# Kernel tuning notes

Hardware: AMD Instinct MI355X
Metric: run time of the kernel (lower is better)

## Reference

```python
import jax, jax.numpy as jnp
import numpy as np

HEAD_NUM = 8
NEG = 10000.0


def setup_inputs() -> dict:
    key = jax.random.key(0)
    ks = jax.random.split(key, 8)
    B, S, D = 2, 2048, 512
    sc = 1.0 / np.sqrt(D)
    return {
        "x": jax.random.normal(ks[0], (B, S, D), dtype=jnp.float32),
        "mask": jax.random.randint(ks[1], (B, S), 0, 2, dtype=jnp.int32),
        "Wq": jax.random.normal(ks[2], (D, D), dtype=jnp.float32) * sc,
        "bq": jnp.zeros((D,), jnp.float32),
        "Wk": jax.random.normal(ks[3], (D, D), dtype=jnp.float32) * sc,
        "bk": jnp.zeros((D,), jnp.float32),
        "Wv": jax.random.normal(ks[4], (D, D), dtype=jnp.float32) * sc,
        "bv": jnp.zeros((D,), jnp.float32),
        "Wo": jax.random.normal(ks[5], (D, D), dtype=jnp.float32) * sc,
        "bo": jnp.zeros((D,), jnp.float32),
    }


def _split_heads(t, H):
    B, S, D = t.shape
    return t.reshape(B, S, H, D // H).transpose(0, 2, 1, 3)  # [B,H,S,hd]


def reference(x, mask, Wq, bq, Wk, bk, Wv, bv, Wo, bo):
    B, S, D = x.shape
    H = HEAD_NUM
    hd = D // H
    # linear projections + relu activation (as in keras layer)
    q = jax.nn.relu(x @ Wq + bq)
    k = jax.nn.relu(x @ Wk + bk)
    v = jax.nn.relu(x @ Wv + bv)
    q = _split_heads(q, H)
    k = _split_heads(k, H)
    v = _split_heads(v, H)
    # scaled dot-product scores: scale by sqrt(head_dim) (query last dim after split)
    e = jnp.einsum("bhqd,bhkd->bhqk", q, k) / jnp.sqrt(jnp.float32(hd))
    # causal (history_only) additive mask
    idx = jnp.arange(S)
    causal = (idx[None, :] > idx[:, None]).astype(jnp.float32)  # [S,S]
    e = e - NEG * causal[None, None, :, :]
    # key padding mask, additive
    e = e - NEG * (1.0 - mask.astype(jnp.float32))[:, None, None, :]
    # stable softmax (explicit max-subtract as in source)
    a = jax.nn.softmax(e, axis=-1)
    out = jnp.einsum("bhqk,bhkd->bhqd", a, v)  # [B,H,S,hd]
    out = out.transpose(0, 2, 1, 3).reshape(B, S, D)
    # output projection + activation
    return jax.nn.relu(out @ Wo + bo)
```

## Files before the change

kernel.cpp:

```cpp
#include <hip/hip_runtime.h>
#include <hip/hip_bf16.h>

constexpr int Bc = 2, Sc = 2048, Dc = 512, Hc = 8, HDc = 64;
constexpr int Mtot = Bc * Sc;
constexpr size_t HEADMAT = (size_t)Bc * Hc * Sc * HDc;
constexpr float SC2  = 0.18033688011112042f;
constexpr float NEG2 = 14426.950408889634f;

typedef __attribute__((ext_vector_type(8)))  short          short8;
typedef __attribute__((ext_vector_type(8)))  unsigned short ushort8;
typedef __attribute__((ext_vector_type(4)))  float          f32x4;
typedef __attribute__((ext_vector_type(16))) float          f32x16;

#define MFMA16 __builtin_amdgcn_mfma_f32_16x16x32_bf16
#define MFMA32 __builtin_amdgcn_mfma_f32_32x32x16_bf16

static __device__ __forceinline__ unsigned short f32_to_bf16_bits(float f) {
    unsigned int u = __builtin_bit_cast(unsigned int, f);
    unsigned int r = u + 0x7FFFu + ((u >> 16) & 1u);
    return (unsigned short)(r >> 16);
}
static __device__ __forceinline__ unsigned int pkbf(float a, float b) {
    return (unsigned int)f32_to_bf16_bits(a) |
           ((unsigned int)f32_to_bf16_bits(b) << 16);
}

__global__ __launch_bounds__(256)
void convert_x(const float* __restrict__ x, unsigned short* __restrict__ Xb, int n)
{
    const int i = (blockIdx.x * 256 + threadIdx.x) * 4;
    if (i >= n) return;
    const float4 v = *(const float4*)(x + i);
    ushort4 o;
    o.x = f32_to_bf16_bits(v.x);
    o.y = f32_to_bf16_bits(v.y);
    o.z = f32_to_bf16_bits(v.z);
    o.w = f32_to_bf16_bits(v.w);
    *(ushort4*)(Xb + i) = o;
}

__global__ __launch_bounds__(256)
void transpose_w(const float* __restrict__ W0, const float* __restrict__ W1,
                 const float* __restrict__ W2, const float* __restrict__ W3,
                 unsigned short* __restrict__ Wt)
{
    __shared__ float T[64][65];
    const int z = blockIdx.z;
    const float* Wp = (z == 0) ? W0 : (z == 1) ? W1 : (z == 2) ? W2 : W3;
    unsigned short* Op = Wt + (size_t)z * 512 * 512;

    const int kt = blockIdx.y * 64, nt = blockIdx.x * 64;
    const int t = threadIdx.x;
    const int r  = t >> 2, c4 = (t & 3) * 16;

    #pragma unroll
    for (int i = 0; i < 4; ++i) {
        const float4 v = *(const float4*)(Wp + (size_t)(kt + r) * 512 + nt + c4 + 4 * i);
        T[r][c4 + 4*i + 0] = v.x;
        T[r][c4 + 4*i + 1] = v.y;
        T[r][c4 + 4*i + 2] = v.z;
        T[r][c4 + 4*i + 3] = v.w;
    }
    __syncthreads();

    const int n = t >> 2, k4 = (t & 3) * 16;
    #pragma unroll
    for (int i = 0; i < 4; ++i) {
        ushort4 o;
        o.x = f32_to_bf16_bits(T[k4 + 4*i + 0][n]);
        o.y = f32_to_bf16_bits(T[k4 + 4*i + 1][n]);
        o.z = f32_to_bf16_bits(T[k4 + 4*i + 2][n]);
        o.w = f32_to_bf16_bits(T[k4 + 4*i + 3][n]);
        *(ushort4*)(Op + (size_t)(nt + n) * 512 + kt + k4 + 4 * i) = o;
    }
}

template<bool HEADOUT>
__global__ __launch_bounds__(256)
void gemm_tile(const unsigned short* __restrict__ Xb,
               const unsigned short* __restrict__ Wt,
               const float* __restrict__ b0, const float* __restrict__ b1,
               const float* __restrict__ b2,
               unsigned short* __restrict__ Hout,
               float* __restrict__ Yf)
{
    __shared__ short As[128 * 32];
    __shared__ short Bs[64 * 32];

    const int lane = threadIdx.x & 63, wave = threadIdx.x >> 6;
    const int c = lane & 15, g = lane >> 4;
    const int wr = wave >> 1, wc = wave & 1;
    const int z = blockIdx.z;
    const unsigned short* Wp = Wt + (size_t)z * 512 * 512;
    const float* bp = (z == 0) ? b0 : (z == 1) ? b1 : b2;
    const int bm = blockIdx.y * 128;
    const int bn = blockIdx.x * 64;

    const int srow = lane >> 2;
    const int scol = (lane & 3) * 8;

    f32x4 acc[4][2] = {};

    for (int k0 = 0; k0 < 512; k0 += 32) {
        __syncthreads();
        #pragma unroll
        for (int i = 0; i < 2; ++i) {
            const int row = (wave * 2 + i) * 16 + srow;
            const short8 v = *(const short8*)(Xb + (size_t)(bm + row) * 512 + k0 + scol);
            *(short8*)(&As[row * 32 + scol]) = v;
        }
        {
            const int row = wave * 16 + srow;
            const short8 v = *(const short8*)(Wp + (size_t)(bn + row) * 512 + k0 + scol);
            *(short8*)(&Bs[row * 32 + scol]) = v;
        }
        __syncthreads();

        short8 a[4], bfr[2];
        #pragma unroll
        for (int mi = 0; mi < 4; ++mi)
            a[mi] = *(const short8*)(&As[(wr * 64 + mi * 16 + c) * 32 + g * 8]);
        #pragma unroll
        for (int ni = 0; ni < 2; ++ni)
            bfr[ni] = *(const short8*)(&Bs[(wc * 32 + ni * 16 + c) * 32 + g * 8]);
        #pragma unroll
        for (int mi = 0; mi < 4; ++mi)
            #pragma unroll
            for (int ni = 0; ni < 2; ++ni)
                acc[mi][ni] = MFMA16(a[mi], bfr[ni], acc[mi][ni], 0, 0, 0);
    }

    #pragma unroll
    for (int mi = 0; mi < 4; ++mi) {
        #pragma unroll
        for (int ni = 0; ni < 2; ++ni) {
            const int n = bn + wc * 32 + ni * 16 + c;
            const float bias = bp[n];
            float v[4];
            #pragma unroll
            for (int r = 0; r < 4; ++r)
                v[r] = fmaxf(acc[mi][ni][r] + bias, 0.0f);
            const int mbase = bm + wr * 64 + mi * 16 + 4 * g;
            if constexpr (HEADOUT) {
                const int bb = mbase >> 11, ss = mbase & 2047;
                const int hh = n >> 6, hd = n & 63;
                if (z == 2) {
                    union { ushort4 u; unsigned short s[4]; } pk;
                    #pragma unroll
                    for (int r = 0; r < 4; ++r) pk.s[r] = f32_to_bf16_bits(v[r]);
                    *reinterpret_cast<ushort4*>(
                        Hout + (size_t)2 * HEADMAT +
                        ((size_t)(bb * Hc + hh) * HDc + hd) * Sc + ss) = pk.u;
                } else {
                    #pragma unroll
                    for (int r = 0; r < 4; ++r)
                        Hout[(size_t)z * HEADMAT +
                             (((size_t)(bb * Hc + hh) * Sc + ss + r) * HDc + hd)] =
                            f32_to_bf16_bits(v[r]);
                }
            } else {
                #pragma unroll
                for (int r = 0; r < 4; ++r)
                    Yf[(size_t)(mbase + r) * 512 + n] = v[r];
            }
        }
    }
}

__global__ __launch_bounds__(256)
void attn_mfma(const short* __restrict__ Qh, const short* __restrict__ Kh,
               const short* __restrict__ Vt, const int* __restrict__ mask,
               unsigned short* __restrict__ Ob)
{
    __shared__ __align__(16) char smem[4 * 8448 + 4 * 256];

    const int lane = threadIdx.x & 63;
    const int wave = threadIdx.x >> 6;
    const int bid  = blockIdx.x;
    const int swz  = (bid & 7) * 128 + (bid >> 3);
    const int t    = swz & 63;
    const int h    = (swz >> 6) & 7;
    const int b    = swz >> 9;
    const int q0   = t * 32;
    const int r32  = lane & 31;
    const int hi   = lane >> 5;

    char*  wreg = smem + wave * 8448;
    float* Lml  = (float*)(smem + 4 * 8448 + wave * 256);

    const size_t headoff = (size_t)(b * Hc + h) * Sc * HDc;
    const short* Qp = Qh + headoff;
    const short* Kp = Kh + headoff;
    const short* Vp = Vt + headoff;
    const int* mb = mask + b * Sc;

    int fb = Sc;
    for (int base = 0; base < Sc; base += 64) {
        unsigned long long bal = __ballot(mb[base + lane] != 0);
        if (bal) { fb = base + (__ffsll(bal) - 1); break; }
    }
    const int kmax = (fb <= q0) ? (q0 + 32) : Sc;
    const int kend = (kmax + 31) & ~31;
    const int nT   = kend >> 5;
    const int tpw  = (nT + 3) >> 2;
    const int kbeg = wave * tpw * 32;
    const int kfin = min(kend, kbeg + tpw * 32);

    short8 qf[4];
    #pragma unroll
    for (int j = 0; j < 4; ++j)
        qf[j] = *(const short8*)(Qp + (size_t)(q0 + r32) * HDc + j * 16 + hi * 8);

    f32x16 acc0 = {0,0,0,0,0,0,0,0,0,0,0,0,0,0,0,0};
    f32x16 acc1 = {0,0,0,0,0,0,0,0,0,0,0,0,0,0,0,0};
    float m = -1e30f, l = 0.0f;

    const short* vrow0 = Vp + (size_t)r32 * Sc + 8 * hi;
    const short* vrow1 = Vp + (size_t)(32 + r32) * Sc + 8 * hi;

    for (int k0 = kbeg; k0 < kfin; k0 += 32) {
        const short8 va0 = *(const short8*)(vrow0 + k0);
        const short8 va1 = *(const short8*)(vrow0 + k0 + 16);
        const short8 vb0 = *(const short8*)(vrow1 + k0);
        const short8 vb1 = *(const short8*)(vrow1 + k0 + 16);

        f32x16 s = {0,0,0,0,0,0,0,0,0,0,0,0,0,0,0,0};
        #pragma unroll
        for (int j = 0; j < 4; ++j) {
            const short8 kf =
                *(const short8*)(Kp + (size_t)(k0 + r32) * HDc + j * 16 + hi * 8);
            s = MFMA32(kf, qf[j], s, 0, 0, 0);
        }

        const unsigned long long bal = __ballot(mb[k0 + r32] != 0);
        const unsigned int mloc = ((unsigned int)bal) >> (4 * hi);

        float e[16];
        float tmax = -1e30f;
        if (k0 + 31 > q0) {
            #pragma unroll
            for (int r = 0; r < 16; ++r) {
                const int cr0 = (r & 3) + 8 * (r >> 2);
                float ev = s[r] * SC2;
                if (!((mloc >> cr0) & 1))            ev -= NEG2;
                if (k0 + cr0 + 4 * hi > q0 + r32)    ev -= NEG2;
                e[r] = ev;
                tmax = fmaxf(tmax, ev);
            }
        } else {
            #pragma unroll
            for (int r = 0; r < 16; ++r) {
                const int cr0 = (r & 3) + 8 * (r >> 2);
                float ev = s[r] * SC2;
                if (!((mloc >> cr0) & 1))            ev -= NEG2;
                e[r] = ev;
                tmax = fmaxf(tmax, ev);
            }
        }
        tmax = fmaxf(tmax, __shfl_xor(tmax, 32));

        if (__any(tmax > m)) {
            const float mn   = fmaxf(m, tmax);
            const float corr = __builtin_exp2f(m - mn);
            m = mn; l *= corr;
            acc0 *= corr;
            acc1 *= corr;
        }

        float ps = 0.f;
        #pragma unroll
        for (int r = 0; r < 16; ++r) {
            e[r] = __builtin_exp2f(e[r] - m);
            ps += e[r];
        }
        l += ps;

        const unsigned int A0 = pkbf(e[0],  e[1]),  B0 = pkbf(e[2],  e[3]);
        const unsigned int C0 = pkbf(e[4],  e[5]),  D0 = pkbf(e[6],  e[7]);
        const unsigned int A1 = pkbf(e[8],  e[9]),  B1 = pkbf(e[10], e[11]);
        const unsigned int C1 = pkbf(e[12], e[13]), D1 = pkbf(e[14], e[15]);
        const unsigned int A0s = (unsigned int)__shfl_xor((int)A0, 32);
        const unsigned int B0s = (unsigned int)__shfl_xor((int)B0, 32);
        const unsigned int C0s = (unsigned int)__shfl_xor((int)C0, 32);
        const unsigned int D0s = (unsigned int)__shfl_xor((int)D0, 32);
        const unsigned int A1s = (unsigned int)__shfl_xor((int)A1, 32);
        const unsigned int B1s = (unsigned int)__shfl_xor((int)B1, 32);
        const unsigned int C1s = (unsigned int)__shfl_xor((int)C1, 32);
        const unsigned int D1s = (unsigned int)__shfl_xor((int)D1, 32);

        union { unsigned int u[4]; short8 s8; } P0, P1;
        P0.u[0] = hi ? C0s : A0;  P0.u[1] = hi ? D0s : B0;
        P0.u[2] = hi ? C0  : A0s; P0.u[3] = hi ? D0  : B0s;
        P1.u[0] = hi ? C1s : A1;  P1.u[1] = hi ? D1s : B1;
        P1.u[2] = hi ? C1  : A1s; P1.u[3] = hi ? D1  : B1s;

        acc0 = MFMA32(va0, P0.s8, acc0, 0, 0, 0);
        acc0 = MFMA32(va1, P1.s8, acc0, 0, 0, 0);
        acc1 = MFMA32(vb0, P0.s8, acc1, 0, 0, 0);
        acc1 = MFMA32(vb1, P1.s8, acc1, 0, 0, 0);
    }

    l += __shfl_xor(l, 32);

    {
        float* Lacc = (float*)wreg;
        #pragma unroll
        for (int r = 0; r < 16; ++r) {
            Lacc[lane * 33 + r]      = acc0[r];
            Lacc[lane * 33 + 16 + r] = acc1[r];
        }
        if (lane < 32) { Lml[lane] = m; Lml[32 + lane] = l; }
    }
    __syncthreads();

    float mu[4], lu[4], M = -1e30f;
    #pragma unroll
    for (int u = 0; u < 4; ++u) {
        const float* LmlU = (const float*)(smem + 4 * 8448 + u * 256);
        mu[u] = LmlU[r32];
        lu[u] = LmlU[32 + r32];
        M = fmaxf(M, mu[u]);
    }
    float wgt[4], L = 0.f;
    #pragma unroll
    for (int u = 0; u < 4; ++u) {
        wgt[u] = __builtin_exp2f(mu[u] - M);
        L += wgt[u] * lu[u];
    }
    const float invL = 1.0f / L;

    #pragma unroll
    for (int jj = 0; jj < 8; ++jj) {
        const int j = wave * 8 + jj;
        float o = 0.f;
        #pragma unroll
        for (int u = 0; u < 4; ++u)
            o += wgt[u] * ((const float*)(smem + u * 8448))[lane * 33 + j];
        const int j16 = j & 15;
        const int d = (j16 & 3) + 8 * (j16 >> 2) + 4 * hi + 32 * (j >> 4);
        Ob[(size_t)(b * Sc + q0 + r32) * Dc + h * HDc + d] =
            f32_to_bf16_bits(o * invL);
    }
}

extern "C" void kernel_launch(void* const* d_in, const int* in_sizes, int n_in,
                              void* d_out, int out_size, void* d_ws, size_t ws_size,
                              hipStream_t stream) {
    const float* x  = (const float*)d_in[0];
    const int* mask = (const int*)d_in[1];
    const float* Wq = (const float*)d_in[2];
    const float* bq = (const float*)d_in[3];
    const float* Wk = (const float*)d_in[4];
    const float* bk = (const float*)d_in[5];
    const float* Wv = (const float*)d_in[6];
    const float* bv = (const float*)d_in[7];
    const float* Wo = (const float*)d_in[8];
    const float* bo = (const float*)d_in[9];
    float* out = (float*)d_out;

    unsigned short* Xb = (unsigned short*)d_ws;
    unsigned short* Wt = Xb + (size_t)Mtot * 512;
    unsigned short* Qh = Wt + (size_t)4 * 512 * 512;
    unsigned short* Kh = Qh + HEADMAT;
    unsigned short* Vt = Kh + HEADMAT;
    unsigned short* Ob = Vt + HEADMAT;

    convert_x<<<dim3((Mtot * 512) / 1024), dim3(256), 0, stream>>>(
        x, Xb, Mtot * 512);
    transpose_w<<<dim3(8, 8, 4), dim3(256), 0, stream>>>(Wq, Wk, Wv, Wo, Wt);
    gemm_tile<true><<<dim3(8, Mtot / 128, 3), dim3(256), 0, stream>>>(
        Xb, Wt, bq, bk, bv, Qh, nullptr);
    attn_mfma<<<dim3(1024), dim3(256), 0, stream>>>(
        (const short*)Qh, (const short*)Kh, (const short*)Vt, mask, Ob);
    gemm_tile<false><<<dim3(8, Mtot / 128, 1), dim3(256), 0, stream>>>(
        Ob, Wt + (size_t)3 * 512 * 512, bo, bo, bo, nullptr, out);
}
```

Measured before the change: 97.49 us.

## Panelize V layout, prescale Q, reverse tile order, use packed bf16 convert

Measured after the change: 92.87 us. 1.05x faster.

```diff
diff --git a/kernel.cpp b/kernel.cpp
--- a/kernel.cpp
+++ b/kernel.cpp
@@ -20,9 +20,10 @@
     unsigned int r = u + 0x7FFFu + ((u >> 16) & 1u);
     return (unsigned short)(r >> 16);
 }
-static __device__ __forceinline__ unsigned int pkbf(float a, float b) {
-    return (unsigned int)f32_to_bf16_bits(a) |
-           ((unsigned int)f32_to_bf16_bits(b) << 16);
+static __device__ __forceinline__ unsigned int pk2bf(float a, float b) {
+    union { __hip_bfloat162 h2; unsigned int u; } cv;
+    cv.h2 = __float22bfloat162_rn(make_float2(a, b));
+    return cv.u;
 }
 
 __global__ __launch_bounds__(256)
@@ -138,8 +139,10 @@
             const float bias = bp[n];
             float v[4];
             #pragma unroll
-            for (int r = 0; r < 4; ++r)
+            for (int r = 0; r < 4; ++r) {
                 v[r] = fmaxf(acc[mi][ni][r] + bias, 0.0f);
+                if (HEADOUT && z == 0) v[r] *= SC2;
+            }
             const int mbase = bm + wr * 64 + mi * 16 + 4 * g;
             if constexpr (HEADOUT) {
                 const int bb = mbase >> 11, ss = mbase & 2047;
@@ -150,7 +153,8 @@
                     for (int r = 0; r < 4; ++r) pk.s[r] = f32_to_bf16_bits(v[r]);
                     *reinterpret_cast<ushort4*>(
                         Hout + (size_t)2 * HEADMAT +
-                        ((size_t)(bb * Hc + hh) * HDc + hd) * Sc + ss) = pk.u;
+                        (size_t)(bb * Hc + hh) * Sc * HDc +
+                        (size_t)(ss >> 5) * (HDc * 32) + hd * 32 + (ss & 31)) = pk.u;
                 } else {
                     #pragma unroll
                     for (int r = 0; r < 4; ++r)
@@ -169,7 +173,7 @@
 
 __global__ __launch_bounds__(256)
 void attn_mfma(const short* __restrict__ Qh, const short* __restrict__ Kh,
-               const short* __restrict__ Vt, const int* __restrict__ mask,
+               const short* __restrict__ Vb, const int* __restrict__ mask,
                unsigned short* __restrict__ Ob)
 {
     __shared__ __align__(16) char smem[4 * 8448 + 4 * 256];
@@ -178,7 +182,7 @@
     const int wave = threadIdx.x >> 6;
     const int bid  = blockIdx.x;
     const int swz  = (bid & 7) * 128 + (bid >> 3);
-    const int t    = swz & 63;
+    const int t    = 63 - (swz & 63);
     const int h    = (swz >> 6) & 7;
     const int b    = swz >> 9;
     const int q0   = t * 32;
@@ -191,7 +195,7 @@
     const size_t headoff = (size_t)(b * Hc + h) * Sc * HDc;
     const short* Qp = Qh + headoff;
     const short* Kp = Kh + headoff;
-    const short* Vp = Vt + headoff;
+    const short* Vp = Vb + headoff;
     const int* mb = mask + b * Sc;
 
     int fb = Sc;
@@ -215,14 +219,15 @@
     f32x16 acc1 = {0,0,0,0,0,0,0,0,0,0,0,0,0,0,0,0};
     float m = -1e30f, l = 0.0f;
 
-    const short* vrow0 = Vp + (size_t)r32 * Sc + 8 * hi;
-    const short* vrow1 = Vp + (size_t)(32 + r32) * Sc + 8 * hi;
+    const int vo0 = r32 * 32 + 8 * hi;
+    const int vo1 = (32 + r32) * 32 + 8 * hi;
 
     for (int k0 = kbeg; k0 < kfin; k0 += 32) {
-        const short8 va0 = *(const short8*)(vrow0 + k0);
-        const short8 va1 = *(const short8*)(vrow0 + k0 + 16);
-        const short8 vb0 = *(const short8*)(vrow1 + k0);
-        const short8 vb1 = *(const short8*)(vrow1 + k0 + 16);
+        const short* vpan = Vp + (size_t)k0 * 64;
+        const short8 va0 = *(const short8*)(vpan + vo0);
+        const short8 va1 = *(const short8*)(vpan + vo0 + 16);
+        const short8 vb0 = *(const short8*)(vpan + vo1);
+        const short8 vb1 = *(const short8*)(vpan + vo1 + 16);
 
         f32x16 s = {0,0,0,0,0,0,0,0,0,0,0,0,0,0,0,0};
         #pragma unroll
@@ -241,7 +246,7 @@
             #pragma unroll
             for (int r = 0; r < 16; ++r) {
                 const int cr0 = (r & 3) + 8 * (r >> 2);
-                float ev = s[r] * SC2;
+                float ev = s[r];
                 if (!((mloc >> cr0) & 1))            ev -= NEG2;
                 if (k0 + cr0 + 4 * hi > q0 + r32)    ev -= NEG2;
                 e[r] = ev;
@@ -251,7 +256,7 @@
             #pragma unroll
             for (int r = 0; r < 16; ++r) {
                 const int cr0 = (r & 3) + 8 * (r >> 2);
-                float ev = s[r] * SC2;
+                float ev = s[r];
                 if (!((mloc >> cr0) & 1))            ev -= NEG2;
                 e[r] = ev;
                 tmax = fmaxf(tmax, ev);
@@ -275,10 +280,10 @@
         }
         l += ps;
 
-        const unsigned int A0 = pkbf(e[0],  e[1]),  B0 = pkbf(e[2],  e[3]);
-        const unsigned int C0 = pkbf(e[4],  e[5]),  D0 = pkbf(e[6],  e[7]);
-        const unsigned int A1 = pkbf(e[8],  e[9]),  B1 = pkbf(e[10], e[11]);
-        const unsigned int C1 = pkbf(e[12], e[13]), D1 = pkbf(e[14], e[15]);
+        const unsigned int A0 = pk2bf(e[0],  e[1]),  B0 = pk2bf(e[2],  e[3]);
+        const unsigned int C0 = pk2bf(e[4],  e[5]),  D0 = pk2bf(e[6],  e[7]);
+        const unsigned int A1 = pk2bf(e[8],  e[9]),  B1 = pk2bf(e[10], e[11]);
+        const unsigned int C1 = pk2bf(e[12], e[13]), D1 = pk2bf(e[14], e[15]);
         const unsigned int A0s = (unsigned int)__shfl_xor((int)A0, 32);
         const unsigned int B0s = (unsigned int)__shfl_xor((int)B0, 32);
         const unsigned int C0s = (unsigned int)__shfl_xor((int)C0, 32);
@@ -362,8 +367,8 @@
     unsigned short* Wt = Xb + (size_t)Mtot * 512;
     unsigned short* Qh = Wt + (size_t)4 * 512 * 512;
     unsigned short* Kh = Qh + HEADMAT;
-    unsigned short* Vt = Kh + HEADMAT;
-    unsigned short* Ob = Vt + HEADMAT;
+    unsigned short* Vb = Kh + HEADMAT;
+    unsigned short* Ob = Vb + HEADMAT;
 
     convert_x<<<dim3((Mtot * 512) / 1024), dim3(256), 0, stream>>>(
         x, Xb, Mtot * 512);
@@ -371,7 +376,7 @@
     gemm_tile<true><<<dim3(8, Mtot / 128, 3), dim3(256), 0, stream>>>(
         Xb, Wt, bq, bk, bv, Qh, nullptr);
     attn_mfma<<<dim3(1024), dim3(256), 0, stream>>>(
-        (const short*)Qh, (const short*)Kh, (const short*)Vt, mask, Ob);
+        (const short*)Qh, (const short*)Kh, (const short*)Vb, mask, Ob);
     gemm_tile<false><<<dim3(8, Mtot / 128, 1), dim3(256), 0, stream>>>(
         Ob, Wt + (size_t)3 * 512 * 512, bo, bo, bo, nullptr, out);
 }
```
